# Optimization experiments

Hardware: AMD Instinct MI355X
Metric: run time of the kernel (lower is better)

## Reference

```python
import jax, jax.numpy as jnp
import numpy as np

ALPHA = 0.1
STEPS = 4


def setup_inputs() -> dict:
    key = jax.random.key(0)
    x = jax.random.normal(key, (4, 8192, 1024), dtype=jnp.float32)
    return {"x": x}


def reference(x) -> jnp.ndarray:
    # CtaPostAttnMixer.forward, layout='bld', prefill, steps=4, alpha=0.1
    # Fixed-boundary 1D heat-diffusion stencil along the sequence dim.
    if x.shape[1] < 3:
        return x
    y = x.astype(jnp.float32)
    for _ in range(STEPS):
        # Laplacian on interior tokens: y[l+1] - 2 y[l] + y[l-1]
        lap = y[:, 2:, :] - 2.0 * y[:, 1:-1, :] + y[:, :-2, :]
        y = jnp.concatenate(
            [y[:, :1, :], y[:, 1:-1, :] + ALPHA * lap, y[:, -1:, :]], axis=1
        )
    return y.astype(x.dtype)
```

## Files before the change

kernel.cpp:

```cpp
#include <hip/hip_runtime.h>


namespace {

constexpr int Lr   = 8192;
constexpr int Dq   = 1024 / 4;
constexpr int Bn   = 4;
constexpr int C    = 4;
constexpr int W    = C + 8;
constexpr int SEGS = Lr / C;

constexpr float WK0 = 0.4870f;
constexpr float WK1 = 0.2144f;
constexpr float WK2 = 0.0388f;
constexpr float WK3 = 0.0032f;
constexpr float WK4 = 0.0001f;

typedef float nfloat4 __attribute__((ext_vector_type(4)));

__device__ __forceinline__ float4 f4_add(float4 a, float4 b) {
    return make_float4(a.x + b.x, a.y + b.y, a.z + b.z, a.w + b.w);
}
__device__ __forceinline__ float4 f4_mul(float s, float4 a) {
    return make_float4(s * a.x, s * a.y, s * a.z, s * a.w);
}
__device__ __forceinline__ float4 f4_fma(float s, float4 a, float4 c) {
    return make_float4(fmaf(s, a.x, c.x), fmaf(s, a.y, c.y),
                       fmaf(s, a.z, c.z), fmaf(s, a.w, c.w));
}
__device__ __forceinline__ void f4_store_nt(float4* p, float4 v) {
    nfloat4 nv;
    nv.x = v.x; nv.y = v.y; nv.z = v.z; nv.w = v.w;
    __builtin_nontemporal_store(nv, (nfloat4*)p);
}

__global__ __launch_bounds__(256, 8)
void mixer4_kernel(const float4* __restrict__ x, float4* __restrict__ y) {
    const int d4  = threadIdx.x;
    const int seg = blockIdx.x;
    const int b   = blockIdx.y;
    const int c0  = seg * C;

    const float4* __restrict__ xb = x + (size_t)b * Lr * Dq + d4;
    float4* __restrict__       yb = y + (size_t)b * Lr * Dq + d4;

    float4 w[W];
#pragma unroll
    for (int i = 0; i < W; ++i) {
        int gl = c0 - 4 + i;
        gl = gl < 0 ? 0 : gl;
        gl = gl > Lr - 1 ? Lr - 1 : gl;
        w[i] = xb[(size_t)gl * Dq];
    }

    if (c0 != 0 && c0 != Lr - C) {
#pragma unroll
        for (int j = 0; j < C; ++j) {
            float4 acc = f4_mul(WK0, w[j + 4]);
            acc = f4_fma(WK1, f4_add(w[j + 3], w[j + 5]), acc);
            acc = f4_fma(WK2, f4_add(w[j + 2], w[j + 6]), acc);
            acc = f4_fma(WK3, f4_add(w[j + 1], w[j + 7]), acc);
            acc = f4_fma(WK4, f4_add(w[j + 0], w[j + 8]), acc);
            f4_store_nt(&yb[(size_t)(c0 + j) * Dq], acc);
        }
    } else if (c0 == 0) {
        f4_store_nt(&yb[0], w[4]);
        {
            float4 o = f4_mul(0.2986f, w[4]);
            o = f4_fma(0.4482f, w[5], o);
            o = f4_fma(0.2112f, w[6], o);
            o = f4_fma(0.0387f, w[7], o);
            o = f4_fma(0.0032f, w[8], o);
            o = f4_fma(0.0001f, w[9], o);
            f4_store_nt(&yb[(size_t)1 * Dq], o);
        }
        {
            float4 o = f4_mul(0.0454f, w[4]);
            o = f4_fma(0.2112f, w[5], o);
            o = f4_fma(0.4869f, w[6], o);
            o = f4_fma(0.2144f, w[7], o);
            o = f4_fma(0.0388f, w[8], o);
            o = f4_fma(0.0032f, w[9], o);
            o = f4_fma(0.0001f, w[10], o);
            f4_store_nt(&yb[(size_t)2 * Dq], o);
        }
        {
            float4 o = f4_mul(0.0034f, w[4]);
            o = f4_fma(0.0387f, w[5], o);
            o = f4_fma(0.2144f, w[6], o);
            o = f4_fma(0.4870f, w[7], o);
            o = f4_fma(0.2144f, w[8], o);
            o = f4_fma(0.0388f, w[9], o);
            o = f4_fma(0.0032f, w[10], o);
            o = f4_fma(0.0001f, w[11], o);
            f4_store_nt(&yb[(size_t)3 * Dq], o);
        }
    } else {
        f4_store_nt(&yb[(size_t)(Lr - 1) * Dq], w[7]);
        {
            float4 o = f4_mul(0.2986f, w[7]);
            o = f4_fma(0.4482f, w[6], o);
            o = f4_fma(0.2112f, w[5], o);
            o = f4_fma(0.0387f, w[4], o);
            o = f4_fma(0.0032f, w[3], o);
            o = f4_fma(0.0001f, w[2], o);
            f4_store_nt(&yb[(size_t)(Lr - 2) * Dq], o);
        }
        {
            float4 o = f4_mul(0.0454f, w[7]);
            o = f4_fma(0.2112f, w[6], o);
            o = f4_fma(0.4869f, w[5], o);
            o = f4_fma(0.2144f, w[4], o);
            o = f4_fma(0.0388f, w[3], o);
            o = f4_fma(0.0032f, w[2], o);
            o = f4_fma(0.0001f, w[1], o);
            f4_store_nt(&yb[(size_t)(Lr - 3) * Dq], o);
        }
        {
            float4 o = f4_mul(0.0034f, w[7]);
            o = f4_fma(0.0387f, w[6], o);
            o = f4_fma(0.2144f, w[5], o);
            o = f4_fma(0.4870f, w[4], o);
            o = f4_fma(0.2144f, w[3], o);
            o = f4_fma(0.0388f, w[2], o);
            o = f4_fma(0.0032f, w[1], o);
            o = f4_fma(0.0001f, w[0], o);
            f4_store_nt(&yb[(size_t)(Lr - 4) * Dq], o);
        }
    }
}

}

extern "C" void kernel_launch(void* const* d_in, const int* in_sizes, int n_in,
                              void* d_out, int out_size, void* d_ws, size_t ws_size,
                              hipStream_t stream) {
    const float4* x = (const float4*)d_in[0];
    float4*       y = (float4*)d_out;

    dim3 grid(SEGS, Bn);
    dim3 block(256);
    hipLaunchKernelGGL(mixer4_kernel, grid, block, 0, stream, x, y);
}
```

Baseline: 230.5 us.

## Tile sequence in LDS with async global-to-LDS loads to cut halo re-reads

Each block now stages a 40-row by 64-float4 slab of the input in LDS and computes 32 output rows, four waves handling eight rows each. Before, every block of four output rows re-read twelve input rows from global memory; now each input row is read about 1.25 times. The LDS fill uses the `__builtin_amdgcn_global_load_lds` direct-to-LDS path when available. In exchange it adds a block barrier, uses more LDS and lowers the occupancy hint. Boundary handling is remapped for the first and last tiles.

```diff
diff --git a/kernel.cpp b/kernel.cpp
--- a/kernel.cpp
+++ b/kernel.cpp
@@ -3,12 +3,14 @@
 
 namespace {
 
-constexpr int Lr   = 8192;
-constexpr int Dq   = 1024 / 4;
-constexpr int Bn   = 4;
-constexpr int C    = 4;
-constexpr int W    = C + 8;
-constexpr int SEGS = Lr / C;
+constexpr int Lr    = 8192;
+constexpr int Dq    = 1024 / 4;
+constexpr int SW    = 64;
+constexpr int NS    = Dq / SW;
+constexpr int Bn    = 4;
+constexpr int TL    = 32;
+constexpr int LDSR  = TL + 8;
+constexpr int TILES = Lr / TL;
 
 constexpr float WK0 = 0.4870f;
 constexpr float WK1 = 0.2144f;
@@ -34,37 +36,67 @@
     __builtin_nontemporal_store(nv, (nfloat4*)p);
 }
 
-__global__ __launch_bounds__(256, 8)
+#if defined(__has_builtin) && __has_builtin(__builtin_amdgcn_global_load_lds)
+#define HAVE_GLL 1
+#else
+#define HAVE_GLL 0
+#endif
+
+__global__ __launch_bounds__(256, 4)
 void mixer4_kernel(const float4* __restrict__ x, float4* __restrict__ y) {
-    const int d4  = threadIdx.x;
-    const int seg = blockIdx.x;
-    const int b   = blockIdx.y;
-    const int c0  = seg * C;
+    __shared__ float4 sm[LDSR * SW];
 
-    const float4* __restrict__ xb = x + (size_t)b * Lr * Dq + d4;
-    float4* __restrict__       yb = y + (size_t)b * Lr * Dq + d4;
+    const int t    = threadIdx.x;
+    const int lane = t & 63;
+    const int wav  = t >> 6;
+    const int tile = blockIdx.x;
+    const int cs   = blockIdx.y;
+    const int b    = blockIdx.z;
+    const int l0   = tile * TL;
 
-    float4 w[W];
+    const float4* __restrict__ xb = x + (size_t)b * Lr * Dq + cs * SW;
+    float4* __restrict__       yb = y + (size_t)b * Lr * Dq + cs * SW;
+
 #pragma unroll
-    for (int i = 0; i < W; ++i) {
-        int gl = c0 - 4 + i;
+    for (int i = 0; i < LDSR / 4; ++i) {
+        int r  = wav * (LDSR / 4) + i;
+        int gl = l0 - 4 + r;
         gl = gl < 0 ? 0 : gl;
         gl = gl > Lr - 1 ? Lr - 1 : gl;
-        w[i] = xb[(size_t)gl * Dq];
+        const float4* src = xb + (size_t)gl * Dq + lane;
+        float4*       dst = &sm[r * SW];
+#if HAVE_GLL
+        __builtin_amdgcn_global_load_lds(
+            (const __attribute__((address_space(1))) void*)src,
+            (__attribute__((address_space(3))) void*)dst, 16, 0, 0);
+#else
+        sm[r * SW + lane] = *src;
+#endif
     }
+    __syncthreads();
 
-    if (c0 != 0 && c0 != Lr - C) {
+    const int c  = lane;
+    const int r0 = wav * 8;
+
+    float4 w[16];
 #pragma unroll
-        for (int j = 0; j < C; ++j) {
+    for (int i = 0; i < 16; ++i) w[i] = sm[(r0 + i) * SW + c];
+
+    const bool first = (tile == 0);
+    const bool last  = (tile == TILES - 1);
+
+    if (!(first && wav == 0) && !(last && wav == 3)) {
+#pragma unroll
+        for (int j = 0; j < 8; ++j) {
             float4 acc = f4_mul(WK0, w[j + 4]);
             acc = f4_fma(WK1, f4_add(w[j + 3], w[j + 5]), acc);
             acc = f4_fma(WK2, f4_add(w[j + 2], w[j + 6]), acc);
             acc = f4_fma(WK3, f4_add(w[j + 1], w[j + 7]), acc);
             acc = f4_fma(WK4, f4_add(w[j + 0], w[j + 8]), acc);
-            f4_store_nt(&yb[(size_t)(c0 + j) * Dq], acc);
+            f4_store_nt(&yb[(size_t)(l0 + r0 + j) * Dq + c], acc);
         }
-    } else if (c0 == 0) {
-        f4_store_nt(&yb[0], w[4]);
+    } else if (first && wav == 0) {
+        f4_store_nt(&yb[0 * Dq + c], w[4]);
         {
             float4 o = f4_mul(0.2986f, w[4]);
             o = f4_fma(0.4482f, w[5], o);
@@ -72,7 +104,7 @@
             o = f4_fma(0.0387f, w[7], o);
             o = f4_fma(0.0032f, w[8], o);
             o = f4_fma(0.0001f, w[9], o);
-            f4_store_nt(&yb[(size_t)1 * Dq], o);
+            f4_store_nt(&yb[(size_t)1 * Dq + c], o);
         }
         {
             float4 o = f4_mul(0.0454f, w[4]);
@@ -82,7 +114,7 @@
             o = f4_fma(0.0388f, w[8], o);
             o = f4_fma(0.0032f, w[9], o);
             o = f4_fma(0.0001f, w[10], o);
-            f4_store_nt(&yb[(size_t)2 * Dq], o);
+            f4_store_nt(&yb[(size_t)2 * Dq + c], o);
         }
         {
             float4 o = f4_mul(0.0034f, w[4]);
@@ -93,39 +125,57 @@
             o = f4_fma(0.0388f, w[9], o);
             o = f4_fma(0.0032f, w[10], o);
             o = f4_fma(0.0001f, w[11], o);
-            f4_store_nt(&yb[(size_t)3 * Dq], o);
+            f4_store_nt(&yb[(size_t)3 * Dq + c], o);
+        }
+#pragma unroll
+        for (int j = 4; j < 8; ++j) {
+            float4 acc = f4_mul(WK0, w[j + 4]);
+            acc = f4_fma(WK1, f4_add(w[j + 3], w[j + 5]), acc);
+            acc = f4_fma(WK2, f4_add(w[j + 2], w[j + 6]), acc);
+            acc = f4_fma(WK3, f4_add(w[j + 1], w[j + 7]), acc);
+            acc = f4_fma(WK4, f4_add(w[j + 0], w[j + 8]), acc);
+            f4_store_nt(&yb[(size_t)j * Dq + c], acc);
         }
     } else {
-        f4_store_nt(&yb[(size_t)(Lr - 1) * Dq], w[7]);
+#pragma unroll
+        for (int j = 0; j < 4; ++j) {
+            float4 acc = f4_mul(WK0, w[j + 4]);
+            acc = f4_fma(WK1, f4_add(w[j + 3], w[j + 5]), acc);
+            acc = f4_fma(WK2, f4_add(w[j + 2], w[j + 6]), acc);
+            acc = f4_fma(WK3, f4_add(w[j + 1], w[j + 7]), acc);
+            acc = f4_fma(WK4, f4_add(w[j + 0], w[j + 8]), acc);
+            f4_store_nt(&yb[(size_t)(l0 + 24 + j) * Dq + c], acc);
+        }
+        f4_store_nt(&yb[(size_t)(Lr - 1) * Dq + c], w[11]);
         {
-            float4 o = f4_mul(0.2986f, w[7]);
-            o = f4_fma(0.4482f, w[6], o);
-            o = f4_fma(0.2112f, w[5], o);
-            o = f4_fma(0.0387f, w[4], o);
-            o = f4_fma(0.0032f, w[3], o);
-            o = f4_fma(0.0001f, w[2], o);
-            f4_store_nt(&yb[(size_t)(Lr - 2) * Dq], o);
+            float4 o = f4_mul(0.2986f, w[11]);
+            o = f4_fma(0.4482f, w[10], o);
+            o = f4_fma(0.2112f, w[9], o);
+            o = f4_fma(0.0387f, w[8], o);
+            o = f4_fma(0.0032f, w[7], o);
+            o = f4_fma(0.0001f, w[6], o);
+            f4_store_nt(&yb[(size_t)(Lr - 2) * Dq + c], o);
         }
         {
-            float4 o = f4_mul(0.0454f, w[7]);
-            o = f4_fma(0.2112f, w[6], o);
-            o = f4_fma(0.4869f, w[5], o);
-            o = f4_fma(0.2144f, w[4], o);
-            o = f4_fma(0.0388f, w[3], o);
-            o = f4_fma(0.0032f, w[2], o);
-            o = f4_fma(0.0001f, w[1], o);
-            f4_store_nt(&yb[(size_t)(Lr - 3) * Dq], o);
+            float4 o = f4_mul(0.0454f, w[11]);
+            o = f4_fma(0.2112f, w[10], o);
+            o = f4_fma(0.4869f, w[9], o);
+            o = f4_fma(0.2144f, w[8], o);
+            o = f4_fma(0.0388f, w[7], o);
+            o = f4_fma(0.0032f, w[6], o);
+            o = f4_fma(0.0001f, w[5], o);
+            f4_store_nt(&yb[(size_t)(Lr - 3) * Dq + c], o);
         }
         {
-            float4 o = f4_mul(0.0034f, w[7]);
-            o = f4_fma(0.0387f, w[6], o);
-            o = f4_fma(0.2144f, w[5], o);
-            o = f4_fma(0.4870f, w[4], o);
-            o = f4_fma(0.2144f, w[3], o);
-            o = f4_fma(0.0388f, w[2], o);
-            o = f4_fma(0.0032f, w[1], o);
-            o = f4_fma(0.0001f, w[0], o);
-            f4_store_nt(&yb[(size_t)(Lr - 4) * Dq], o);
+            float4 o = f4_mul(0.0034f, w[11]);
+            o = f4_fma(0.0387f, w[10], o);
+            o = f4_fma(0.2144f, w[9], o);
+            o = f4_fma(0.4870f, w[8], o);
+            o = f4_fma(0.2144f, w[7], o);
+            o = f4_fma(0.0388f, w[6], o);
+            o = f4_fma(0.0032f, w[5], o);
+            o = f4_fma(0.0001f, w[4], o);
+            f4_store_nt(&yb[(size_t)(Lr - 4) * Dq + c], o);
         }
     }
 }
@@ -138,7 +188,7 @@
     const float4* x = (const float4*)d_in[0];
     float4*       y = (float4*)d_out;
 
-    dim3 grid(SEGS, Bn);
+    dim3 grid(TILES, NS, Bn);
     dim3 block(256);
     hipLaunchKernelGGL(mixer4_kernel, grid, block, 0, stream, x, y);
 }
```

After: 241.8 us. +4.9%, slower.
